# Kernel tuning notes

Hardware: AMD Instinct MI355X
Metric: run time of the kernel (lower is better)

Reference implementation:

```python
import jax, jax.numpy as jnp
import numpy as np

R_MIN, R_MAX, THETA_MAX = 0.4, 0.99, 6.283185307179586
ORDER = 64  # K = order//2 = 32 pole pairs


def setup_inputs() -> dict:
    key = jax.random.key(0)
    k1, k2, k3, k4, k5 = jax.random.split(key, 5)
    K, D = ORDER // 2, 1024
    u1 = jax.random.uniform(k1, (K, D), dtype=jnp.float32)
    u2 = jax.random.uniform(k2, (K, D), dtype=jnp.float32)
    scale = np.sqrt(2.0 / ORDER).astype(np.float32)
    return {
        "r": R_MIN + (R_MAX - R_MIN) * u1,                         # pole radii
        "theta": THETA_MAX * u2,                                    # pole angles
        "R_re": jax.random.normal(k3, (K, D), dtype=jnp.float32) * scale,
        "R_im": jax.random.normal(k4, (K, D), dtype=jnp.float32) * scale,
        "h_0": jax.random.normal(k5, (1, D), dtype=jnp.float32),
        "L": 2048,
    }


def reference(r, theta, R_re, R_im, h_0, L):
    # poles p = r * exp(i*theta), residues R = R_re + i*R_im; shapes (K, D)
    p = r.astype(jnp.complex64) * jnp.exp(1j * theta.astype(jnp.complex64))
    R = R_re + 1j * R_im                                            # (K, D) complex64
    t = jnp.arange(L - 1, dtype=jnp.float32)[:, None, None]         # (L-1, 1, 1)
    # h[t, d] = Re( sum_k R[k,d] * p[k,d]^t )
    h = jnp.sum(R[None] * p[None] ** t, axis=1).real                # (L-1, D)
    h = jnp.concatenate([h_0, h], axis=0)                           # (L, D)
    return h.T                                                      # (D, L)
```

## Files before the change

### kernel.cpp

```cpp
#include <hip/hip_runtime.h>


#define KP 32
#define KP2 16
#define DD 1024
#define LL 2048
#define INV_2PI 0x1.45f306p-3f

typedef float v2f __attribute__((ext_vector_type(2)));

__global__ __launch_bounds__(256) void modal_filter_kernel(
    const float* __restrict__ r, const float* __restrict__ theta,
    const float* __restrict__ Rre, const float* __restrict__ Rim,
    const float* __restrict__ h0, float* __restrict__ out) {
  const int d = blockIdx.x;
  const int tid = threadIdx.x;

  __shared__ float s_lr[KP];
  __shared__ float s_thr[KP];
  __shared__ float s_qre[KP];
  __shared__ float s_qim[KP];
  __shared__ float s_Rre[KP];
  __shared__ float s_Rim[KP];

  if (tid < KP) {
    const float rv = r[tid * DD + d];
    const float th = theta[tid * DD + d];
    const float lr = __builtin_amdgcn_logf(rv);
    const float thr = th * INV_2PI;
    const float qmag = __builtin_amdgcn_exp2f(256.0f * lr);
    const float qang = __builtin_amdgcn_fractf(256.0f * thr);
    s_lr[tid] = lr;
    s_thr[tid] = thr;
    s_qre[tid] = qmag * __builtin_amdgcn_cosf(qang);
    s_qim[tid] = qmag * __builtin_amdgcn_sinf(qang);
    s_Rre[tid] = Rre[tid * DD + d];
    s_Rim[tid] = Rim[tid * DD + d];
  }
  __syncthreads();

  v2f ZRE[KP2], ZIM[KP2], QRE[KP2], QIM[KP2];
  const float t0 = (float)tid - 1.0f;
#pragma unroll
  for (int kk = 0; kk < KP2; ++kk) {
#pragma unroll
    for (int j = 0; j < 2; ++j) {
      const int k = 2 * kk + j;
      const float mag = __builtin_amdgcn_exp2f(t0 * s_lr[k]);
      const float ang = __builtin_amdgcn_fractf(t0 * s_thr[k]);
      const float c = __builtin_amdgcn_cosf(ang);
      const float s = __builtin_amdgcn_sinf(ang);
      const float wre = mag * c, wim = mag * s;
      ZRE[kk][j] = s_Rre[k] * wre - s_Rim[k] * wim;
      ZIM[kk][j] = s_Rre[k] * wim + s_Rim[k] * wre;
      QRE[kk][j] = s_qre[k];
      QIM[kk][j] = s_qim[k];
    }
  }

  float* outd = out + (size_t)d * LL;
  const float h0d = h0[d];

#pragma unroll
  for (int s = 0; s < 8; ++s) {
    v2f a0 = {0.f, 0.f}, a1 = {0.f, 0.f}, a2 = {0.f, 0.f}, a3 = {0.f, 0.f};
#pragma unroll
    for (int kk = 0; kk < KP2; kk += 4) {
      a0 += ZRE[kk];
      a1 += ZRE[kk + 1];
      a2 += ZRE[kk + 2];
      a3 += ZRE[kk + 3];
    }
    const v2f aa = (a0 + a1) + (a2 + a3);
    const float acc = aa[0] + aa[1];
    const int l = tid + 256 * s;
    outd[l] = (l == 0) ? h0d : acc;
    if (s < 7) {
#pragma unroll
      for (int kk = 0; kk < KP2; ++kk) {
        const v2f nr = ZRE[kk] * QRE[kk] - ZIM[kk] * QIM[kk];
        const v2f ni = ZRE[kk] * QIM[kk] + ZIM[kk] * QRE[kk];
        ZRE[kk] = nr;
        ZIM[kk] = ni;
      }
    }
  }
}

extern "C" void kernel_launch(void* const* d_in, const int* in_sizes, int n_in,
                              void* d_out, int out_size, void* d_ws, size_t ws_size,
                              hipStream_t stream) {
  const float* r     = (const float*)d_in[0];
  const float* theta = (const float*)d_in[1];
  const float* Rre   = (const float*)d_in[2];
  const float* Rim   = (const float*)d_in[3];
  const float* h0    = (const float*)d_in[4];
  float* out = (float*)d_out;

  modal_filter_kernel<<<DD, 256, 0, stream>>>(r, theta, Rre, Rim, h0, out);
}
```

Baseline: 73.49 us.

## Halve block size and broadcast pole params via readlane instead of LDS

Each wavefront now loads the 32 pole parameters directly (one per lane) and broadcasts them with readlane, removing the shared-memory staging and the block barrier. The block size drops from 256 to 128 threads, so each thread runs 16 recurrence steps instead of 8, with a step multiplier of p^128. The aim is less setup overhead per thread and no synchronisation, in exchange for more serial complex multiplies per thread and longer recurrence chains, which may add rounding error.

Measured after the change: 73.52 us. About the same (+0.0%).

```diff
diff --git a/kernel.cpp b/kernel.cpp
--- a/kernel.cpp
+++ b/kernel.cpp
@@ -5,64 +5,60 @@
 #define KP2 16
 #define DD 1024
 #define LL 2048
+#define TPB 128
+#define NS (LL / TPB)
 #define INV_2PI 0x1.45f306p-3f
 
 typedef float v2f __attribute__((ext_vector_type(2)));
 
-__global__ __launch_bounds__(256) void modal_filter_kernel(
+__device__ __forceinline__ float rdlane(float x, int k) {
+  return __int_as_float(__builtin_amdgcn_readlane(__float_as_int(x), k));
+}
+
+__global__ __launch_bounds__(TPB) void modal_filter_kernel(
     const float* __restrict__ r, const float* __restrict__ theta,
     const float* __restrict__ Rre, const float* __restrict__ Rim,
     const float* __restrict__ h0, float* __restrict__ out) {
   const int d = blockIdx.x;
   const int tid = threadIdx.x;
+  const int lane = tid & 63;
 
-  __shared__ float s_lr[KP];
-  __shared__ float s_thr[KP];
-  __shared__ float s_qre[KP];
-  __shared__ float s_qim[KP];
-  __shared__ float s_Rre[KP];
-  __shared__ float s_Rim[KP];
-
-  if (tid < KP) {
-    const float rv = r[tid * DD + d];
-    const float th = theta[tid * DD + d];
-    const float lr = __builtin_amdgcn_logf(rv);
-    const float thr = th * INV_2PI;
-    const float qmag = __builtin_amdgcn_exp2f(256.0f * lr);
-    const float qang = __builtin_amdgcn_fractf(256.0f * thr);
-    s_lr[tid] = lr;
-    s_thr[tid] = thr;
-    s_qre[tid] = qmag * __builtin_amdgcn_cosf(qang);
-    s_qim[tid] = qmag * __builtin_amdgcn_sinf(qang);
-    s_Rre[tid] = Rre[tid * DD + d];
-    s_Rim[tid] = Rim[tid * DD + d];
-  }
-  __syncthreads();
+  const int j = lane & (KP - 1);
+  const float rv   = r[j * DD + d];
+  const float th   = theta[j * DD + d];
+  const float Rrev = Rre[j * DD + d];
+  const float Rimv = Rim[j * DD + d];
+  const float lr  = __builtin_amdgcn_logf(rv);
+  const float thr = th * INV_2PI;
+  const float qmag = __builtin_amdgcn_exp2f((float)TPB * lr);
+  const float qang = __builtin_amdgcn_fractf((float)TPB * thr);
+  const float qreL = qmag * __builtin_amdgcn_cosf(qang);
+  const float qimL = qmag * __builtin_amdgcn_sinf(qang);
 
   v2f ZRE[KP2], ZIM[KP2], QRE[KP2], QIM[KP2];
   const float t0 = (float)tid - 1.0f;
 #pragma unroll
-  for (int kk = 0; kk < KP2; ++kk) {
-#pragma unroll
-    for (int j = 0; j < 2; ++j) {
-      const int k = 2 * kk + j;
-      const float mag = __builtin_amdgcn_exp2f(t0 * s_lr[k]);
-      const float ang = __builtin_amdgcn_fractf(t0 * s_thr[k]);
-      const float c = __builtin_amdgcn_cosf(ang);
-      const float s = __builtin_amdgcn_sinf(ang);
-      const float wre = mag * c, wim = mag * s;
-      ZRE[kk][j] = s_Rre[k] * wre - s_Rim[k] * wim;
-      ZIM[kk][j] = s_Rre[k] * wim + s_Rim[k] * wre;
-      QRE[kk][j] = s_qre[k];
-      QIM[kk][j] = s_qim[k];
-    }
+  for (int k = 0; k < KP; ++k) {
+    const float plr  = rdlane(lr, k);
+    const float pthr = rdlane(thr, k);
+    const float pRre = rdlane(Rrev, k);
+    const float pRim = rdlane(Rimv, k);
+    const float mag = __builtin_amdgcn_exp2f(t0 * plr);
+    const float ang = __builtin_amdgcn_fractf(t0 * pthr);
+    const float c = __builtin_amdgcn_cosf(ang);
+    const float s = __builtin_amdgcn_sinf(ang);
+    const float wre = mag * c, wim = mag * s;
+    ZRE[k >> 1][k & 1] = pRre * wre - pRim * wim;
+    ZIM[k >> 1][k & 1] = pRre * wim + pRim * wre;
+    QRE[k >> 1][k & 1] = rdlane(qreL, k);
+    QIM[k >> 1][k & 1] = rdlane(qimL, k);
   }
 
   float* outd = out + (size_t)d * LL;
   const float h0d = h0[d];
 
 #pragma unroll
-  for (int s = 0; s < 8; ++s) {
+  for (int s = 0; s < NS; ++s) {
     v2f a0 = {0.f, 0.f}, a1 = {0.f, 0.f}, a2 = {0.f, 0.f}, a3 = {0.f, 0.f};
 #pragma unroll
     for (int kk = 0; kk < KP2; kk += 4) {
@@ -73,9 +69,9 @@
     }
     const v2f aa = (a0 + a1) + (a2 + a3);
     const float acc = aa[0] + aa[1];
-    const int l = tid + 256 * s;
+    const int l = tid + TPB * s;
     outd[l] = (l == 0) ? h0d : acc;
-    if (s < 7) {
+    if (s < NS - 1) {
 #pragma unroll
       for (int kk = 0; kk < KP2; ++kk) {
         const v2f nr = ZRE[kk] * QRE[kk] - ZIM[kk] * QIM[kk];
@@ -97,5 +93,5 @@
   const float* h0    = (const float*)d_in[4];
   float* out = (float*)d_out;
 
-  modal_filter_kernel<<<DD, 256, 0, stream>>>(r, theta, Rre, Rim, h0, out);
+  modal_filter_kernel<<<DD, TPB, 0, stream>>>(r, theta, Rre, Rim, h0, out);
 }
```
